# Kernel optimization log

Measured on AMD Instinct MI355X. Metric: run time of the kernel, lower is better.

Reference implementation:

```python
import jax, jax.numpy as jnp
import numpy as np

D_MODEL = 768
HEADS = 12
D_HEAD = D_MODEL // HEADS
D_DYNA = 768
EPS = 1e-5
B, SP, SI = 16, 256, 1024


def _layernorm(x, g, b):
    mu = jnp.mean(x, axis=-1, keepdims=True)
    var = jnp.var(x, axis=-1, keepdims=True)
    return (x - mu) * jax.lax.rsqrt(var + EPS) * g + b


def _mha(q, k, v, wq, bq, wk, bk, wv, bv, wo, bo):
    # weights stored [d_in, d_out]; torch Linear math y = x @ W^T + b is
    # equivalent with transposed storage.
    B_ = q.shape[0]
    qh = (q @ wq + bq).reshape(B_, -1, HEADS, D_HEAD)
    kh = (k @ wk + bk).reshape(B_, -1, HEADS, D_HEAD)
    vh = (v @ wv + bv).reshape(B_, -1, HEADS, D_HEAD)
    scores = jnp.einsum('bqhd,bkhd->bhqk', qh, kh) / np.sqrt(D_HEAD).astype(np.float32)
    attn = jax.nn.softmax(scores, axis=-1)  # dropout disabled (eval)
    out = jnp.einsum('bhqk,bkhd->bqhd', attn, vh).reshape(B_, -1, D_MODEL)
    return out @ wo + bo


def setup_inputs() -> dict:
    key = jax.random.key(0)
    ks = iter(jax.random.split(key, 40))
    s = 0.02
    d = {
        'image': jax.random.normal(next(ks), (B, SI, D_MODEL), jnp.float32),
        'prompt': jax.random.normal(next(ks), (B, SP, D_MODEL), jnp.float32),
        'posi': jax.random.normal(next(ks), (B, SI, D_MODEL), jnp.float32),
        'posp': jax.random.normal(next(ks), (B, SP, D_MODEL), jnp.float32),
    }
    for ln in ('ln_p1', 'ln_p2', 'ln_p3', 'ln_i1'):
        d[ln + '_g'] = jnp.ones((D_MODEL,), jnp.float32)
        d[ln + '_b'] = jnp.zeros((D_MODEL,), jnp.float32)
    for pre in ('pp', 'pi'):
        for nm in ('q', 'k', 'v', 'o'):
            d[f'{pre}_w{nm}'] = s * jax.random.normal(next(ks), (D_MODEL, D_MODEL), jnp.float32)
            d[f'{pre}_b{nm}'] = jnp.zeros((D_MODEL,), jnp.float32)
    d['ff_w1'] = s * jax.random.normal(next(ks), (D_MODEL, D_MODEL), jnp.float32)
    d['ff_b1'] = jnp.zeros((D_MODEL,), jnp.float32)
    d['ff_w2'] = s * jax.random.normal(next(ks), (D_MODEL, D_DYNA), jnp.float32)
    d['ff_b2'] = jnp.zeros((D_DYNA,), jnp.float32)
    return d


def reference(image, prompt, posi, posp,
              ln_p1_g, ln_p1_b, ln_p2_g, ln_p2_b, ln_p3_g, ln_p3_b, ln_i1_g, ln_i1_b,
              pp_wq, pp_bq, pp_wk, pp_bk, pp_wv, pp_bv, pp_wo, pp_bo,
              pi_wq, pi_bq, pi_wk, pi_bk, pi_wv, pi_bv, pi_wo, pi_bo,
              ff_w1, ff_b1, ff_w2, ff_b2):
    prompt0 = prompt + posp
    xp = _layernorm(prompt0, ln_p1_g, ln_p1_b)
    xp = _mha(xp, xp, xp, pp_wq, pp_bq, pp_wk, pp_bk, pp_wv, pp_bv, pp_wo, pp_bo)
    prompt = prompt + xp  # dropout_p1 is identity in eval
    xp = _layernorm(prompt + prompt0, ln_p2_g, ln_p2_b)
    xi = _layernorm(image + posi, ln_i1_g, ln_i1_b)
    xp = _mha(xp, xi, xi, pi_wq, pi_bq, pi_wk, pi_bk, pi_wv, pi_bv, pi_wo, pi_bo)
    prompt = prompt + xp  # dropout_p2 identity
    xp = _layernorm(prompt + prompt0, ln_p3_g, ln_p3_b)
    xp = jax.nn.relu(xp @ ff_w1 + ff_b1) @ ff_w2 + ff_b2
    return xp
```

## Files before the change

### kernel.cpp

```cpp
#include <hip/hip_runtime.h>
#include <hip/hip_bf16.h>
#include <stdint.h>
#include <math.h>

#define D_MODEL 768
#define HEADS 12
#define D_HEAD 64
#define BATCH 16
#define SP 256
#define SI 1024
#define NP (BATCH * SP)
#define NI (BATCH * SI)

#define GLOBAL_AS __attribute__((address_space(1)))
#define LDS_AS    __attribute__((address_space(3)))

typedef __attribute__((ext_vector_type(8))) short  frag_ab;
typedef __attribute__((ext_vector_type(4))) float  frag_cd;

static __device__ __forceinline__ ushort f2bf(float f) {
  __hip_bfloat16 h = __float2bfloat16(f);
  return *(ushort*)&h;
}
static __device__ __forceinline__ float bf2f(ushort u) {
  return __bfloat162float(*(__hip_bfloat16*)&u);
}
static __device__ __forceinline__ bool probe_bf(const uint32_t* p) {
  return p[0] == 0x3F803F80u;
}

struct Prep {
  const void* wsrc[10]; ushort* wdst[10];
  const void* vsrc[18]; float* vdst;
};

__global__ __launch_bounds__(256) void prep_kernel(Prep p, const uint32_t* probe) {
  const bool isbf = probe_bf(probe);
  const int z = blockIdx.z;
  if (z < 10) {
    __shared__ float tile[32][33];
    const int tx = threadIdx.x & 31, ty = threadIdx.x >> 5;
    const int x0 = blockIdx.x * 32, y0 = blockIdx.y * 32;
    const void* src = p.wsrc[z];
    ushort* dst = p.wdst[z];
#pragma unroll
    for (int i = 0; i < 4; i++) {
      const int y = y0 + ty + i * 8;
      float v;
      if (isbf) v = bf2f(((const ushort*)src)[(size_t)y * 768 + x0 + tx]);
      else      v = ((const float*)src)[(size_t)y * 768 + x0 + tx];
      tile[ty + i * 8][tx] = v;
    }
    __syncthreads();
#pragma unroll
    for (int i = 0; i < 4; i++) {
      const int row = x0 + ty + i * 8;
      const int col = y0 + tx;
      dst[(size_t)row * 768 + col] = f2bf(tile[tx][ty + i * 8]);
    }
  } else {
    const int idx = (blockIdx.y * 24 + blockIdx.x) * 256 + threadIdx.x;
    if (idx < 18 * 768) {
      const int e = idx / 768, i = idx - e * 768;
      float v;
      if (isbf) v = bf2f(((const ushort*)p.vsrc[e])[i]);
      else      v = ((const float*)p.vsrc[e])[i];
      p.vdst[idx] = v;
    }
  }
}

struct LNJob {
  const void* a; const void* b;
  const float* g; const float* be;
  float* sum_out; ushort* ln_out;
  int nrows; int abf;
};

__global__ __launch_bounds__(256) void add_ln_wave(LNJob J0, LNJob J1, const uint32_t* probe) {
  const int w = threadIdx.x >> 6, lane = threadIdx.x & 63;
  int row = blockIdx.x * 4 + w;
  LNJob j = (row < J0.nrows) ? J0 : J1;
  if (row >= J0.nrows) row -= J0.nrows;
  if (row >= j.nrows) return;
  const size_t base = (size_t)row * D_MODEL;
  const bool isbf = j.abf && probe_bf(probe);
  float x[12];
#pragma unroll
  for (int k = 0; k < 3; k++) {
    const int c = k * 256 + lane * 4;
    if (isbf) {
      const uint2 ua = *(const uint2*)((const ushort*)j.a + base + c);
      const uint2 ub = *(const uint2*)((const ushort*)j.b + base + c);
      const ushort* pa = (const ushort*)&ua;
      const ushort* pb = (const ushort*)&ub;
#pragma unroll
      for (int t = 0; t < 4; t++) x[k * 4 + t] = bf2f(pa[t]) + bf2f(pb[t]);
    } else {
      const float4 fa = *(const float4*)((const float*)j.a + base + c);
      const float4 fb = *(const float4*)((const float*)j.b + base + c);
      x[k * 4 + 0] = fa.x + fb.x; x[k * 4 + 1] = fa.y + fb.y;
      x[k * 4 + 2] = fa.z + fb.z; x[k * 4 + 3] = fa.w + fb.w;
    }
    if (j.sum_out) {
      float4 s4;
      s4.x = x[k * 4 + 0]; s4.y = x[k * 4 + 1];
      s4.z = x[k * 4 + 2]; s4.w = x[k * 4 + 3];
      *(float4*)&j.sum_out[base + c] = s4;
    }
  }
  float s = 0.f, q = 0.f;
#pragma unroll
  for (int t = 0; t < 12; t++) { s += x[t]; q += x[t] * x[t]; }
#pragma unroll
  for (int o = 32; o > 0; o >>= 1) { s += __shfl_xor(s, o); q += __shfl_xor(q, o); }
  const float mu  = s * (1.0f / D_MODEL);
  const float var = q * (1.0f / D_MODEL) - mu * mu;
  const float inv = rsqrtf(var + 1e-5f);
#pragma unroll
  for (int k = 0; k < 3; k++) {
    const int c = k * 256 + lane * 4;
    const float4 gv = *(const float4*)&j.g[c];
    const float4 bv = *(const float4*)&j.be[c];
    uint2 ou;
    ushort* oe = (ushort*)&ou;
    oe[0] = f2bf((x[k * 4 + 0] - mu) * inv * gv.x + bv.x);
    oe[1] = f2bf((x[k * 4 + 1] - mu) * inv * gv.y + bv.y);
    oe[2] = f2bf((x[k * 4 + 2] - mu) * inv * gv.z + bv.z);
    oe[3] = f2bf((x[k * 4 + 3] - mu) * inv * gv.w + bv.w);
    *(uint2*)(j.ln_out + base + c) = ou;
  }
}

#define BAR   __builtin_amdgcn_s_barrier()
#define LGKM0 do { asm volatile("s_waitcnt lgkmcnt(0)" ::: "memory"); \
                   __builtin_amdgcn_sched_barrier(0); } while (0)
#define VMC4  do { asm volatile("s_waitcnt vmcnt(4)" ::: "memory"); \
                   __builtin_amdgcn_sched_barrier(0); } while (0)

#define RD_A(SL) do { \
  const ushort* _b = &lds[SL][0][0]; \
  _Pragma("unroll") for (int _m = 0; _m < 4; ++_m) \
  _Pragma("unroll") for (int _k = 0; _k < 2; ++_k) \
    aF[_m][_k] = *(const frag_ab*)(_b + ((wr << 6) + _m * 16 + ml) * 64 + \
                                   (((_k << 5) + (kq << 3)) ^ swz)); \
} while (0)

#define RD_B(DST, SL, no) do { \
  const ushort* _b = &lds[SL][1][0]; \
  _Pragma("unroll") for (int _n = 0; _n < 2; ++_n) \
  _Pragma("unroll") for (int _k = 0; _k < 2; ++_k) \
    DST[_n][_k] = *(const frag_ab*)(_b + ((wc << 6) + (no) + _n * 16 + ml) * 64 + \
                                    (((_k << 5) + (kq << 3)) ^ swz)); \
} while (0)

#define MM(NB, BF) do { \
  __builtin_amdgcn_s_setprio(1); \
  _Pragma("unroll") for (int _m = 0; _m < 4; ++_m) \
  _Pragma("unroll") for (int _n = 0; _n < 2; ++_n) \
  _Pragma("unroll") for (int _k = 0; _k < 2; ++_k) \
    acc[_m][(NB) + _n] = __builtin_amdgcn_mfma_f32_16x16x32_bf16( \
        aF[_m][_k], BF[_n][_k], acc[_m][(NB) + _n], 0, 0, 0); \
  __builtin_amdgcn_s_setprio(0); \
} while (0)

#define STAGE(SL, RG, PTR, RBASE, KT) do { \
  const ushort* _p = (PTR) + (size_t)((RBASE) + srow) * 768 + ((KT) << 6) + scol; \
  _Pragma("unroll") for (int _j = 0; _j < 4; ++_j) \
    __builtin_amdgcn_global_load_lds( \
        (const GLOBAL_AS void*)(_p + (size_t)(_j * 32) * 768), \
        (LDS_AS void*)((LDS_AS ushort*)&lds[SL][RG][0] + (((_j << 2) + w) << 9)), \
        16, 0, 0); \
} while (0)

#define ENGINE128() do { \
  STAGE(0, 0, jA, m0, 0); \
  STAGE(0, 1, jB, n0, 0); \
  STAGE(1, 0, jA, m0, 1); \
  VMC4; BAR; \
  for (int it = 0; it < 6; ++it) { \
    const int t1  = 2 * it + 1; \
    const int tn0 = (2 * it + 2 < 12) ? 2 * it + 2 : 11; \
    const int tn1 = (2 * it + 3 < 12) ? 2 * it + 3 : 11; \
     \
    RD_A(0); RD_B(bF0, 0, 0); \
    STAGE(1, 1, jB, n0, t1); \
    LGKM0; \
    MM(0, bF0); \
    BAR; \
     \
    RD_B(bF1, 0, 32); \
    STAGE(0, 0, jA, m0, tn0); \
    LGKM0; \
    MM(2, bF1); \
    VMC4; BAR; \
     \
    RD_A(1); RD_B(bF0, 1, 0); \
    STAGE(0, 1, jB, n0, tn0); \
    LGKM0; \
    MM(0, bF0); \
    BAR; \
     \
    RD_B(bF1, 1, 32); \
    STAGE(1, 0, jA, m0, tn1); \
    LGKM0; \
    MM(2, bF1); \
    VMC4; BAR; \
  } \
} while (0)

struct GJob {
  const ushort* A; const ushort* Bt; const float* bias;
  ushort* o0; ushort* o1; ushort* vT;
  int X; int vsub; int shift;
};

__global__ __launch_bounds__(256, 2) void gemm_mega128(GJob J0, GJob J1, int n0blocks) {
  __shared__ __align__(16) ushort lds[2][2][8192];
  int bid = blockIdx.x;
  GJob j = (bid < n0blocks) ? J0 : J1;
  if (bid >= n0blocks) bid -= n0blocks;
  const int tid  = threadIdx.x;
  const int lane = tid & 63, w = tid >> 6;
  const int wr = w >> 1, wc = w & 1;
  const int ml = lane & 15, kq = lane >> 4;
  const int rest = bid >> 3;
  const int x = rest % j.X, y = (bid & 7) + 8 * (rest / j.X);
  const int m0 = y << 7, n0 = x << 7;
  const int srow = (w << 3) + (lane >> 3);
  const int scol = (((lane & 7) ^ (lane >> 3)) << 3);
  const int swz  = (ml & 7) << 3;
  const ushort* jA = j.A;
  const ushort* jB = j.Bt;

  frag_cd acc[4][4] = {};
  frag_ab aF[4][2], bF0[2][2], bF1[2][2];

  ENGINE128();

  const int sub  = x / 6;
  const int mask = (1 << j.shift) - 1;
#pragma unroll
  for (int mt = 0; mt < 4; mt++) {
#pragma unroll
    for (int nt = 0; nt < 4; nt++) {
      const int row0 = m0 + wr * 64 + mt * 16 + kq * 4;
      const int col  = n0 + wc * 64 + nt * 16 + ml;
      const float bc = j.bias[col];
      if (sub == j.vsub) {
        const int hcol = col - sub * 768;
        const int hh = hcol >> 6, dd = hcol & 63;
        const int bb = row0 >> j.shift;
        const int jj = row0 & mask;
        uint2 pack;
        ushort* pe = (ushort*)&pack;
#pragma unroll
        for (int r = 0; r < 4; r++) pe[r] = f2bf(acc[mt][nt][r] + bc);
        *(uint2*)(j.vT + ((((size_t)(bb * HEADS + hh) << 6) + dd) << j.shift) + jj) = pack;
      } else {
        ushort* out = (sub == 0) ? j.o0 : j.o1;
        const int cl = col - sub * 768;
#pragma unroll
        for (int r = 0; r < 4; r++)
          out[(size_t)(row0 + r) * 768 + cl] = f2bf(acc[mt][nt][r] + bc);
      }
    }
  }
}

__global__ __launch_bounds__(256, 2) void gemm_v3(
    const ushort* __restrict__ A, const ushort* __restrict__ Bt,
    const float* __restrict__ bias,
    const void* __restrict__ resid, int rmode,
    void* __restrict__ C, int relu, int omode,
    const uint32_t* __restrict__ probe, int X) {
  __shared__ __align__(16) ushort lds[2][2][8192];
  const int bid = blockIdx.x;
  const int tid  = threadIdx.x;
  const int lane = tid & 63, w = tid >> 6;
  const int wr = w >> 1, wc = w & 1;
  const int ml = lane & 15, kq = lane >> 4;
  const int rest = bid >> 3;
  const int x = rest % X, y = (bid & 7) + 8 * (rest / X);
  const int m0 = y << 7, n0 = x << 7;
  const int srow = (w << 3) + (lane >> 3);
  const int scol = (((lane & 7) ^ (lane >> 3)) << 3);
  const int swz  = (ml & 7) << 3;
  const ushort* jA = A;
  const ushort* jB = Bt;

  frag_cd acc[4][4] = {};
  frag_ab aF[4][2], bF0[2][2], bF1[2][2];

  ENGINE128();

  const bool obf = (omode == 1) || (omode == 2 && probe_bf(probe));
  const bool rbf = (rmode == 2) && probe_bf(probe);
#pragma unroll
  for (int mt = 0; mt < 4; mt++) {
#pragma unroll
    for (int nt = 0; nt < 4; nt++) {
      const int row0 = m0 + wr * 64 + mt * 16 + kq * 4;
      const int col  = n0 + wc * 64 + nt * 16 + ml;
      const float bc = bias[col];
#pragma unroll
      for (int r = 0; r < 4; r++) {
        const size_t off = (size_t)(row0 + r) * 768 + col;
        float v = acc[mt][nt][r] + bc;
        if (rmode != 0)
          v += rbf ? bf2f(((const ushort*)resid)[off]) : ((const float*)resid)[off];
        if (relu) v = fmaxf(v, 0.f);
        if (obf) ((ushort*)C)[off] = f2bf(v);
        else     ((float*)C)[off]  = v;
      }
    }
  }
}

#undef RD_A
#undef RD_B
#undef MM
#undef STAGE
#undef ENGINE128

#define FS 68
__global__ __launch_bounds__(256) void fattn_mfma(
    const ushort* __restrict__ Q, const ushort* __restrict__ Kp,
    const ushort* __restrict__ vT, ushort* __restrict__ O, int Skv) {
  __shared__ __align__(16) ushort Qs[64 * FS];
  __shared__ __align__(16) ushort Ks[2][64 * FS];
  __shared__ __align__(16) ushort Vt[2][64 * FS];
  __shared__ __align__(16) ushort Ps[64 * FS];
  const int tid  = threadIdx.x;
  const int lane = tid & 63, w = tid >> 6;
  const int ml   = lane & 15, kq = lane >> 4;
  const int bid = blockIdx.x;
  const int g8  = bid & 7;
  const int qt  = (bid >> 3) & 3;
  const int g   = (bid >> 5) * 8 + g8;
  const int h   = g % HEADS;
  const int b   = g / HEADS;
  const int q0  = qt * 64;
  const ushort* Qb  = Q  + ((size_t)b * SP + q0) * D_MODEL + h * D_HEAD;
  const ushort* Kb  = Kp + (size_t)b * Skv * D_MODEL + h * D_HEAD;
  const ushort* vTb = vT + (size_t)g * 64 * Skv;

  const int r0 = tid >> 3, p0 = tid & 7;
  const int r1 = r0 + 32;

  for (int c = tid; c < 512; c += 256) {
    const int r = c >> 3, p = c & 7;
    *(uint4*)&Qs[r * FS + p * 8] = *(const uint4*)(Qb + (size_t)r * D_MODEL + p * 8);
  }

  uint4 kr0 = *(const uint4*)(Kb + (size_t)r0 * D_MODEL + p0 * 8);
  uint4 vr0 = *(const uint4*)(vTb + (size_t)r0 * Skv + p0 * 8);
  uint4 kr1 = *(const uint4*)(Kb + (size_t)r1 * D_MODEL + p0 * 8);
  uint4 vr1 = *(const uint4*)(vTb + (size_t)r1 * Skv + p0 * 8);
  *(uint4*)&Ks[0][r0 * FS + p0 * 8] = kr0;
  *(uint4*)&Vt[0][r0 * FS + p0 * 8] = vr0;
  *(uint4*)&Ks[0][r1 * FS + p0 * 8] = kr1;
  *(uint4*)&Vt[0][r1 * FS + p0 * 8] = vr1;
  __syncthreads();

  frag_ab qa[2];
#pragma unroll
  for (int kc = 0; kc < 2; kc++)
    qa[kc] = *(const frag_ab*)&Qs[(w * 16 + ml) * FS + kc * 32 + kq * 8];

  frag_cd oc[4] = {};
  float m_i[4], l_i[4];
#pragma unroll
  for (int r = 0; r < 4; r++) { m_i[r] = -1e30f; l_i[r] = 0.f; }
  const float SCL = 0.125f * 1.44269504f;
  const int NT = Skv >> 6;

  for (int t = 0; t < NT; ++t) {
    const int cb = t & 1;
    if (t + 1 < NT) {
      const int jn = (t + 1) << 6;
      kr0 = *(const uint4*)(Kb + (size_t)(jn + r0) * D_MODEL + p0 * 8);
      vr0 = *(const uint4*)(vTb + (size_t)r0 * Skv + jn + p0 * 8);
      kr1 = *(const uint4*)(Kb + (size_t)(jn + r1) * D_MODEL + p0 * 8);
      vr1 = *(const uint4*)(vTb + (size_t)r1 * Skv + jn + p0 * 8);
    }

    frag_cd sc[4] = {};
#pragma unroll
    for (int nt = 0; nt < 4; nt++)
#pragma unroll
      for (int kc = 0; kc < 2; kc++) {
        const frag_ab bfr = *(const frag_ab*)&Ks[cb][(nt * 16 + ml) * FS + kc * 32 + kq * 8];
        sc[nt] = __builtin_amdgcn_mfma_f32_16x16x32_bf16(qa[kc], bfr, sc[nt], 0, 0, 0);
      }
#pragma unroll
    for (int nt = 0; nt < 4; nt++)
#pragma unroll
      for (int r = 0; r < 4; r++) sc[nt][r] *= SCL;

    float al[4];
#pragma unroll
    for (int r = 0; r < 4; r++) {
      float mx = fmaxf(fmaxf(sc[0][r], sc[1][r]), fmaxf(sc[2][r], sc[3][r]));
#pragma unroll
      for (int m = 1; m < 16; m <<= 1) mx = fmaxf(mx, __shfl_xor(mx, m, 16));
      const float mnew = fmaxf(m_i[r], mx);
      al[r] = exp2f(m_i[r] - mnew);
      float p[4], s = 0.f;
#pragma unroll
      for (int nt = 0; nt < 4; nt++) { p[nt] = exp2f(sc[nt][r] - mnew); s += p[nt]; }
#pragma unroll
      for (int m = 1; m < 16; m <<= 1) s += __shfl_xor(s, m, 16);
      l_i[r] = l_i[r] * al[r] + s;
      m_i[r] = mnew;
      const int prow = (w * 16 + kq * 4 + r) * FS;
#pragma unroll
      for (int nt = 0; nt < 4; nt++) Ps[prow + nt * 16 + ml] = f2bf(p[nt]);
    }
#pragma unroll
    for (int dt = 0; dt < 4; dt++)
#pragma unroll
      for (int r = 0; r < 4; r++) oc[dt][r] *= al[r];

#pragma unroll
    for (int kc = 0; kc < 2; kc++) {
      const frag_ab pa = *(const frag_ab*)&Ps[(w * 16 + ml) * FS + kc * 32 + kq * 8];
#pragma unroll
      for (int dt = 0; dt < 4; dt++) {
        const frag_ab vb = *(const frag_ab*)&Vt[cb][(dt * 16 + ml) * FS + kc * 32 + kq * 8];
        oc[dt] = __builtin_amdgcn_mfma_f32_16x16x32_bf16(pa, vb, oc[dt], 0, 0, 0);
      }
    }

    if (t + 1 < NT) {
      *(uint4*)&Ks[cb ^ 1][r0 * FS + p0 * 8] = kr0;
      *(uint4*)&Vt[cb ^ 1][r0 * FS + p0 * 8] = vr0;
      *(uint4*)&Ks[cb ^ 1][r1 * FS + p0 * 8] = kr1;
      *(uint4*)&Vt[cb ^ 1][r1 * FS + p0 * 8] = vr1;
      __syncthreads();
    }
  }

  float inv[4];
#pragma unroll
  for (int r = 0; r < 4; r++) inv[r] = 1.0f / l_i[r];
#pragma unroll
  for (int dt = 0; dt < 4; dt++)
#pragma unroll
    for (int r = 0; r < 4; r++)
      O[((size_t)b * SP + q0 + w * 16 + kq * 4 + r) * D_MODEL + h * D_HEAD + dt * 16 + ml] =
          f2bf(oc[dt][r] * inv[r]);
}

extern "C" void kernel_launch(void* const* d_in, const int* in_sizes, int n_in,
                              void* d_out, int out_size, void* d_ws, size_t ws_size,
                              hipStream_t stream) {
  (void)in_sizes; (void)n_in; (void)out_size;
  char* base = (char*)d_ws;
  size_t off = 256;
  auto alloc = [&](size_t bytes) -> char* {
    char* p = base + off;
    off = (off + bytes + 255) & ~(size_t)255;
    return p;
  };
  const size_t WB = (size_t)768 * 768 * 2;
  ushort* Wt[10];
  for (int i = 0; i < 10; i++) Wt[i] = (ushort*)alloc(WB);
  float* vecs = (float*)alloc(18 * 768 * 4);
  float* biasF[10];
  for (int i = 0; i < 10; i++) biasF[i] = vecs + i * 768;
  float* lnF = vecs + 10 * 768;
  float* prompt0 = (float*)alloc((size_t)NP * 768 * 4);
  float* cur     = (float*)alloc((size_t)NP * 768 * 4);
  ushort* q_bf   = (ushort*)alloc((size_t)NP * 768 * 2);
  ushort* k_s    = (ushort*)alloc((size_t)NP * 768 * 2);
  ushort* k_c    = (ushort*)alloc((size_t)NI * 768 * 2);
  ushort* xln_bf = (ushort*)alloc((size_t)NP * 768 * 2);
  ushort* xi_bf  = (ushort*)alloc((size_t)NI * 768 * 2);
  ushort* obuf_bf = (ushort*)alloc((size_t)NP * 768 * 2);
  ushort* ffn1_bf = (ushort*)alloc((size_t)NP * 768 * 2);
  ushort* vT_s   = (ushort*)alloc((size_t)BATCH * HEADS * 64 * SP * 2);
  ushort* vT_c   = (ushort*)alloc((size_t)BATCH * HEADS * 64 * SI * 2);
  if (ws_size < off) return;

  const uint32_t* probe = (const uint32_t*)d_in[4];
  const int widx[10] = {12, 14, 16, 18, 20, 22, 24, 26, 28, 30};
  const int bidx[10] = {13, 15, 17, 19, 21, 23, 25, 27, 29, 31};

  Prep pr{};
  for (int i = 0; i < 10; i++) { pr.wsrc[i] = d_in[widx[i]]; pr.wdst[i] = Wt[i]; }
  for (int i = 0; i < 10; i++) pr.vsrc[i] = d_in[bidx[i]];
  for (int i = 0; i < 8;  i++) pr.vsrc[10 + i] = d_in[4 + i];
  pr.vdst = vecs;
  prep_kernel<<<dim3(24, 24, 11), 256, 0, stream>>>(pr, probe);

  float* G1 = lnF + 0 * 768, *B1 = lnF + 1 * 768;
  float* G2 = lnF + 2 * 768, *B2 = lnF + 3 * 768;
  float* G3 = lnF + 4 * 768, *B3 = lnF + 5 * 768;
  float* Gi = lnF + 6 * 768, *Bi = lnF + 7 * 768;

  LNJob L0{d_in[1], d_in[3], G1, B1, prompt0, xln_bf, NP, 1};
  LNJob Li{d_in[0], d_in[2], Gi, Bi, nullptr, xi_bf,  NI, 1};
  add_ln_wave<<<(NP + NI) / 4, 256, 0, stream>>>(L0, Li, probe);

  GJob js{xln_bf, Wt[0], biasF[0], q_bf, k_s, vT_s, 18, 2, 8};
  GJob jc{xi_bf,  Wt[5], biasF[5], k_c,  nullptr, vT_c, 12, 1, 10};
  gemm_mega128<<<576 + 1536, 256, 0, stream>>>(js, jc, 576);

  fattn_mfma<<<BATCH * HEADS * (SP / 64), 256, 0, stream>>>(q_bf, k_s, vT_s, obuf_bf, SP);

  gemm_v3<<<192, 256, 0, stream>>>(obuf_bf, Wt[3], biasF[3],
      d_in[1], 2, cur, 0, 0, probe, 6);

  LNJob L2{cur, prompt0, G2, B2, nullptr, xln_bf, NP, 0};
  LNJob Lz{}; Lz.nrows = 0;
  add_ln_wave<<<NP / 4, 256, 0, stream>>>(L2, Lz, probe);

  gemm_v3<<<192, 256, 0, stream>>>(xln_bf, Wt[4], biasF[4],
      nullptr, 0, q_bf, 0, 1, probe, 6);

  fattn_mfma<<<BATCH * HEADS * (SP / 64), 256, 0, stream>>>(q_bf, k_c, vT_c, obuf_bf, SI);

  gemm_v3<<<192, 256, 0, stream>>>(obuf_bf, Wt[7], biasF[7],
      cur, 1, cur, 0, 0, probe, 6);

  LNJob L3{cur, prompt0, G3, B3, nullptr, xln_bf, NP, 0};
  add_ln_wave<<<NP / 4, 256, 0, stream>>>(L3, Lz, probe);

  gemm_v3<<<192, 256, 0, stream>>>(xln_bf, Wt[8], biasF[8],
      nullptr, 0, ffn1_bf, 1, 1, probe, 6);

  gemm_v3<<<192, 256, 0, stream>>>(ffn1_bf, Wt[9], biasF[9],
      nullptr, 0, d_out, 0, 2, probe, 6);
}
```

Measured before the change: 504.1 us.

## Replace prompt-side GEMM with 8-wave, 4-stage pipelined 128x128 kernel

```diff
diff --git a/kernel.cpp b/kernel.cpp
--- a/kernel.cpp
+++ b/kernel.cpp
@@ -137,6 +137,8 @@
                    __builtin_amdgcn_sched_barrier(0); } while (0)
 #define VMC4  do { asm volatile("s_waitcnt vmcnt(4)" ::: "memory"); \
                    __builtin_amdgcn_sched_barrier(0); } while (0)
+#define VMC8  do { asm volatile("s_waitcnt vmcnt(8)" ::: "memory"); \
+                   __builtin_amdgcn_sched_barrier(0); } while (0)
 
 #define RD_A(SL) do { \
   const ushort* _b = &lds[SL][0][0]; \
@@ -182,25 +184,21 @@
     const int t1  = 2 * it + 1; \
     const int tn0 = (2 * it + 2 < 12) ? 2 * it + 2 : 11; \
     const int tn1 = (2 * it + 3 < 12) ? 2 * it + 3 : 11; \
-     \
     RD_A(0); RD_B(bF0, 0, 0); \
     STAGE(1, 1, jB, n0, t1); \
     LGKM0; \
     MM(0, bF0); \
     BAR; \
-     \
     RD_B(bF1, 0, 32); \
     STAGE(0, 0, jA, m0, tn0); \
     LGKM0; \
     MM(2, bF1); \
     VMC4; BAR; \
-     \
     RD_A(1); RD_B(bF0, 1, 0); \
     STAGE(0, 1, jB, n0, tn0); \
     LGKM0; \
     MM(0, bF0); \
     BAR; \
-     \
     RD_B(bF1, 1, 32); \
     STAGE(1, 0, jA, m0, tn1); \
     LGKM0; \
@@ -268,17 +266,57 @@
   }
 }
 
-__global__ __launch_bounds__(256, 2) void gemm_v3(
+#undef RD_A
+#undef RD_B
+#undef MM
+#undef STAGE
+#undef ENGINE128
+
+#define DRD_A(SL) do { \
+  const ushort* _b = &lds[SL][0][0]; \
+  _Pragma("unroll") for (int _m = 0; _m < 4; ++_m) \
+  _Pragma("unroll") for (int _k = 0; _k < 2; ++_k) \
+    aF[_m][_k] = *(const frag_ab*)(_b + ((wr << 6) + _m * 16 + ml) * 64 + \
+                                   (((_k << 5) + (kq << 3)) ^ swz)); \
+} while (0)
+
+#define DRD_B(SL) do { \
+  const ushort* _b = &lds[SL][1][0]; \
+  _Pragma("unroll") for (int _n = 0; _n < 2; ++_n) \
+  _Pragma("unroll") for (int _k = 0; _k < 2; ++_k) \
+    bF[_n][_k] = *(const frag_ab*)(_b + ((wc << 5) + _n * 16 + ml) * 64 + \
+                                   (((_k << 5) + (kq << 3)) ^ swz)); \
+} while (0)
+
+#define DMM() do { \
+  __builtin_amdgcn_s_setprio(1); \
+  _Pragma("unroll") for (int _m = 0; _m < 4; ++_m) \
+  _Pragma("unroll") for (int _n = 0; _n < 2; ++_n) \
+  _Pragma("unroll") for (int _k = 0; _k < 2; ++_k) \
+    acc[_m][_n] = __builtin_amdgcn_mfma_f32_16x16x32_bf16( \
+        aF[_m][_k], bF[_n][_k], acc[_m][_n], 0, 0, 0); \
+  __builtin_amdgcn_s_setprio(0); \
+} while (0)
+
+#define DSTG(SL, RG, PTR, RBASE, KT) do { \
+  const ushort* _p = (PTR) + (size_t)((RBASE) + srow) * 768 + ((KT) << 6) + scol; \
+  __builtin_amdgcn_global_load_lds((const GLOBAL_AS void*)_p, \
+      (LDS_AS void*)((LDS_AS ushort*)&lds[SL][RG][0] + (w << 9)), 16, 0, 0); \
+  __builtin_amdgcn_global_load_lds((const GLOBAL_AS void*)(_p + (size_t)64 * 768), \
+      (LDS_AS void*)((LDS_AS ushort*)&lds[SL][RG][0] + ((8 + w) << 9)), 16, 0, 0); \
+} while (0)
+
+__global__ __launch_bounds__(512, 1) void gemm_v3d(
     const ushort* __restrict__ A, const ushort* __restrict__ Bt,
     const float* __restrict__ bias,
     const void* __restrict__ resid, int rmode,
     void* __restrict__ C, int relu, int omode,
     const uint32_t* __restrict__ probe, int X) {
-  __shared__ __align__(16) ushort lds[2][2][8192];
-  const int bid = blockIdx.x;
+  __shared__ __align__(16) ushort lds[4][2][8192];
+  const int bid  = blockIdx.x;
   const int tid  = threadIdx.x;
   const int lane = tid & 63, w = tid >> 6;
-  const int wr = w >> 1, wc = w & 1;
+  const int wr = w >> 2, wc = w & 3;
   const int ml = lane & 15, kq = lane >> 4;
   const int rest = bid >> 3;
   const int x = rest % X, y = (bid & 7) + 8 * (rest / X);
@@ -286,22 +324,36 @@
   const int srow = (w << 3) + (lane >> 3);
   const int scol = (((lane & 7) ^ (lane >> 3)) << 3);
   const int swz  = (ml & 7) << 3;
-  const ushort* jA = A;
-  const ushort* jB = Bt;
-
-  frag_cd acc[4][4] = {};
-  frag_ab aF[4][2], bF0[2][2], bF1[2][2];
-
-  ENGINE128();
+
+  frag_cd acc[4][2] = {};
+  frag_ab aF[4][2], bF[2][2];
+
+  DSTG(0, 0, A, m0, 0); DSTG(0, 1, Bt, n0, 0);
+  DSTG(1, 0, A, m0, 1); DSTG(1, 1, Bt, n0, 1);
+  DSTG(2, 0, A, m0, 2); DSTG(2, 1, Bt, n0, 2);
+  VMC8; BAR;
+
+#pragma unroll 4
+  for (int t = 0; t < 12; ++t) {
+    const int sl  = t & 3;
+    const int tn  = (t + 3 < 12) ? t + 3 : 11;
+    const int sln = (t + 3) & 3;
+    DSTG(sln, 0, A, m0, tn); DSTG(sln, 1, Bt, n0, tn);
+    VMC8;
+    DRD_A(sl); DRD_B(sl);
+    LGKM0;
+    DMM();
+    BAR;
+  }
 
   const bool obf = (omode == 1) || (omode == 2 && probe_bf(probe));
   const bool rbf = (rmode == 2) && probe_bf(probe);
 #pragma unroll
   for (int mt = 0; mt < 4; mt++) {
 #pragma unroll
-    for (int nt = 0; nt < 4; nt++) {
+    for (int nt = 0; nt < 2; nt++) {
       const int row0 = m0 + wr * 64 + mt * 16 + kq * 4;
-      const int col  = n0 + wc * 64 + nt * 16 + ml;
+      const int col  = n0 + wc * 32 + nt * 16 + ml;
       const float bc = bias[col];
 #pragma unroll
       for (int r = 0; r < 4; r++) {
@@ -317,11 +369,10 @@
   }
 }
 
-#undef RD_A
-#undef RD_B
-#undef MM
-#undef STAGE
-#undef ENGINE128
+#undef DRD_A
+#undef DRD_B
+#undef DMM
+#undef DSTG
 
 #define FS 68
 __global__ __launch_bounds__(256) void fattn_mfma(
@@ -509,27 +560,27 @@
 
   fattn_mfma<<<BATCH * HEADS * (SP / 64), 256, 0, stream>>>(q_bf, k_s, vT_s, obuf_bf, SP);
 
-  gemm_v3<<<192, 256, 0, stream>>>(obuf_bf, Wt[3], biasF[3],
+  gemm_v3d<<<192, 512, 0, stream>>>(obuf_bf, Wt[3], biasF[3],
       d_in[1], 2, cur, 0, 0, probe, 6);
 
   LNJob L2{cur, prompt0, G2, B2, nullptr, xln_bf, NP, 0};
   LNJob Lz{}; Lz.nrows = 0;
   add_ln_wave<<<NP / 4, 256, 0, stream>>>(L2, Lz, probe);
 
-  gemm_v3<<<192, 256, 0, stream>>>(xln_bf, Wt[4], biasF[4],
+  gemm_v3d<<<192, 512, 0, stream>>>(xln_bf, Wt[4], biasF[4],
       nullptr, 0, q_bf, 0, 1, probe, 6);
 
   fattn_mfma<<<BATCH * HEADS * (SP / 64), 256, 0, stream>>>(q_bf, k_c, vT_c, obuf_bf, SI);
 
-  gemm_v3<<<192, 256, 0, stream>>>(obuf_bf, Wt[7], biasF[7],
+  gemm_v3d<<<192, 512, 0, stream>>>(obuf_bf, Wt[7], biasF[7],
       cur, 1, cur, 0, 0, probe, 6);
 
   LNJob L3{cur, prompt0, G3, B3, nullptr, xln_bf, NP, 0};
   add_ln_wave<<<NP / 4, 256, 0, stream>>>(L3, Lz, probe);
 
-  gemm_v3<<<192, 256, 0, stream>>>(xln_bf, Wt[8], biasF[8],
+  gemm_v3d<<<192, 512, 0, stream>>>(xln_bf, Wt[8], biasF[8],
       nullptr, 0, ffn1_bf, 1, 1, probe, 6);
 
-  gemm_v3<<<192, 256, 0, stream>>>(ffn1_bf, Wt[9], biasF[9],
+  gemm_v3d<<<192, 512, 0, stream>>>(ffn1_bf, Wt[9], biasF[9],
       nullptr, 0, d_out, 0, 2, probe, 6);
 }
```

Measured after the change: 467.7 us. 7.2% less time.
